# Optimization experiments

Hardware: AMD Instinct MI355X
Metric: run time of the kernel (lower is better)

## Reference

```python
import jax, jax.numpy as jnp
import numpy as np
import math

B, S, OBS, ACT = 64, 256, 96, 29
D, H, L, FF = 512, 8, 8, 2048
HD = D // H
EPS = 1e-5

def _ln(x, g, b):
    m = jnp.mean(x, axis=-1, keepdims=True)
    v = jnp.mean((x - m) ** 2, axis=-1, keepdims=True)
    return (x - m) * jax.lax.rsqrt(v + EPS) * g + b

def _pos_encoding():
    pos = jnp.arange(S, dtype=jnp.float32)[:, None]
    div = jnp.exp(jnp.arange(0, D, 2, dtype=jnp.float32) * (-math.log(10000.0) / D))
    pe = jnp.zeros((S, D), dtype=jnp.float32)
    pe = pe.at[:, 0::2].set(jnp.sin(pos * div))
    pe = pe.at[:, 1::2].set(jnp.cos(pos * div))
    return pe

def setup_inputs() -> dict:
    key = jax.random.key(0)
    ks = iter(jax.random.split(key, 64))
    def w(shape, scale=0.02):
        return jax.random.normal(next(ks), shape, dtype=jnp.float32) * scale
    inp = {
        "observations": jax.random.normal(next(ks), (B, S, OBS), dtype=jnp.float32),
        "W_in": w((OBS, D)), "b_in": jnp.zeros((D,)),
        "g_in": jnp.ones((D,)), "be_in": jnp.zeros((D,)),
        "Wq": w((L, D, D)), "bq": jnp.zeros((L, D)),
        "Wk": w((L, D, D)), "bk": jnp.zeros((L, D)),
        "Wv": w((L, D, D)), "bv": jnp.zeros((L, D)),
        "Wo": w((L, D, D)), "bo": jnp.zeros((L, D)),
        "g1": jnp.ones((L, D)), "be1": jnp.zeros((L, D)),
        "W1": w((L, D, FF)), "b1": jnp.zeros((L, FF)),
        "W2": w((L, FF, D)), "b2": jnp.zeros((L, D)),
        "g2": jnp.ones((L, D)), "be2": jnp.zeros((L, D)),
        "Wp1": w((D, D // 2)), "bp1": jnp.zeros((D // 2,)),
        "gp1": jnp.ones((D // 2,)), "bep1": jnp.zeros((D // 2,)),
        "Wp2": w((D // 2, D // 4)), "bp2": jnp.zeros((D // 4,)),
        "gp2": jnp.ones((D // 4,)), "bep2": jnp.zeros((D // 4,)),
        "Wp3": w((D // 4, ACT)), "bp3": jnp.zeros((ACT,)),
        "action_scale": jnp.ones((ACT,)), "action_bias": jnp.zeros((ACT,)),
    }
    return inp

def _forward(observations, W_in, b_in, g_in, be_in, Wq, bq, Wk, bk, Wv, bv, Wo, bo,
             g1, be1, W1, b1, W2, b2, g2, be2,
             Wp1, bp1, gp1, bep1, Wp2, bp2, gp2, bep2, Wp3, bp3,
             action_scale, action_bias):
    gelu = lambda x: jax.nn.gelu(x, approximate=False)
    # input projection + LN + GELU (dropout = identity in eval)
    x = gelu(_ln(observations @ W_in + b_in, g_in, be_in))
    x = x + _pos_encoding()[None, :, :]  # [B,S,D]
    scale = 1.0 / math.sqrt(HD)
    for l in range(L):
        q = (x @ Wq[l] + bq[l]).reshape(B, S, H, HD)
        k = (x @ Wk[l] + bk[l]).reshape(B, S, H, HD)
        v = (x @ Wv[l] + bv[l]).reshape(B, S, H, HD)
        scores = jnp.einsum('bqhd,bkhd->bhqk', q, k) * scale
        attn = jax.nn.softmax(scores, axis=-1)
        o = jnp.einsum('bhqk,bkhd->bqhd', attn, v).reshape(B, S, D)
        x = _ln(x + (o @ Wo[l] + bo[l]), g1[l], be1[l])
        h = gelu(x @ W1[l] + b1[l])
        x = _ln(x + (h @ W2[l] + b2[l]), g2[l], be2[l])
    y = gelu(_ln(x @ Wp1 + bp1, gp1, bep1))
    y = gelu(_ln(y @ Wp2 + bp2, gp2, bep2))
    actions = jnp.tanh(y @ Wp3 + bp3)
    return actions * action_scale + action_bias

def reference(observations, W_in, b_in, g_in, be_in, Wq, bq, Wk, bk, Wv, bv, Wo, bo,
              g1, be1, W1, b1, W2, b2, g2, be2,
              Wp1, bp1, gp1, bep1, Wp2, bp2, gp2, bep2, Wp3, bp3,
              action_scale, action_bias):
    return _forward(observations, W_in, b_in, g_in, be_in, Wq, bq, Wk, bk, Wv, bv, Wo, bo,
                    g1, be1, W1, b1, W2, b2, g2, be2,
                    Wp1, bp1, gp1, bep1, Wp2, bp2, gp2, bep2, Wp3, bp3,
                    action_scale, action_bias)
```

## Files before the change

### kernel.cpp

```cpp
#include <hip/hip_runtime.h>

typedef unsigned short u16;
typedef unsigned int u32;
typedef __attribute__((ext_vector_type(8))) __bf16 bf16x8;
typedef __attribute__((ext_vector_type(4))) float f32x4;
typedef __attribute__((ext_vector_type(2))) float f32x2;

#define B_ 64
#define S_ 256
#define OBS_ 96
#define ACT_ 29
#define D_ 512
#define H_ 8
#define L_ 8
#define FF_ 2048
#define HD_ 64
#define NTOK (B_ * S_)
#define QKV3 (3 * D_)

__device__ __forceinline__ u16 f2bf(float f) {
    __bf16 h = (__bf16)f;
    u16 u; __builtin_memcpy(&u, &h, 2); return u;
}
__device__ __forceinline__ float bf2f(u16 h) {
    return __uint_as_float(((u32)h) << 16);
}
__device__ __forceinline__ u16 f2h(float f) {
    _Float16 h = (_Float16)f;
    u16 u; __builtin_memcpy(&u, &h, 2); return u;
}
__device__ __forceinline__ float h2f(u16 u) {
    _Float16 h; __builtin_memcpy(&h, &u, 2); return (float)h;
}
__device__ __forceinline__ float gelu_f(float x) {
    const float k1 = 2.3022121f;
    const float k2 = 0.10294451f;
    float x2 = x * x;
    float arg = x * __builtin_fmaf(x2, k2, k1);
    float e = exp2f(arg);
    float r = __builtin_amdgcn_rcpf(1.0f + e);
    return __builtin_fmaf(-x, r, x);
}
__device__ __forceinline__ f32x2 gelu2(f32x2 x) {
    const float k1 = 2.3022121f;
    const float k2 = 0.10294451f;
    f32x2 x2 = x * x;
    f32x2 arg = x * (x2 * k2 + k1);
    f32x2 e;
    e.x = exp2f(arg.x);
    e.y = exp2f(arg.y);
    f32x2 one_e = e + 1.0f;
    f32x2 r;
    r.x = __builtin_amdgcn_rcpf(one_e.x);
    r.y = __builtin_amdgcn_rcpf(one_e.y);
    return x - x * r;
}
__device__ __forceinline__ void gld_lds16(const u16* g, u16* l) {
    __builtin_amdgcn_global_load_lds(
        (const __attribute__((address_space(1))) unsigned int*)g,
        (__attribute__((address_space(3))) unsigned int*)l, 16, 0, 0);
}

__global__ __launch_bounds__(256) void transpose_bf16_kernel(
    const float* __restrict__ src, u16* __restrict__ dst, int K, int N,
    size_t srcStride, size_t dstStride)
{
    __shared__ float tile[32][33];
    int n0 = blockIdx.x * 32, k0 = blockIdx.y * 32;
    const float* s = src + (size_t)blockIdx.z * srcStride;
    u16* d = dst + (size_t)blockIdx.z * dstStride;
    int tx = threadIdx.x, ty = threadIdx.y;
    for (int i = 0; i < 32; i += 8)
        tile[ty + i][tx] = s[(size_t)(k0 + ty + i) * N + n0 + tx];
    __syncthreads();
    for (int i = 0; i < 32; i += 8)
        d[(size_t)(n0 + ty + i) * K + k0 + tx] = f2bf(tile[tx][ty + i]);
}

__global__ __launch_bounds__(256) void concat_bias_kernel(
    const float* __restrict__ bq, const float* __restrict__ bk,
    const float* __restrict__ bv, float* __restrict__ dst)
{
    int i = blockIdx.x * 256 + threadIdx.x;
    int l = i / QKV3, r = i - l * QKV3;
    float v;
    if (r < D_)            v = bq[l * D_ + r];
    else if (r < 2 * D_)   v = bk[l * D_ + r - D_];
    else                   v = bv[l * D_ + r - 2 * D_];
    dst[i] = v;
}

__global__ __launch_bounds__(256) void in_gemm_kernel(
    const float* __restrict__ obs, const float* __restrict__ Win,
    const float* __restrict__ b_in, float* __restrict__ outp)
{
    __shared__ float As[OBS_][68];
    __shared__ float Bs[OBS_][68];
    int m0 = blockIdx.y * 64, n0 = blockIdx.x * 64;
    int t = threadIdx.x;
    #pragma unroll
    for (int i = 0; i < 24; i++) {
        int idx = i * 256 + t;
        int m = idx / OBS_, kk = idx - m * OBS_;
        As[kk][m] = obs[(size_t)(m0 + m) * OBS_ + kk];
    }
    #pragma unroll
    for (int i = 0; i < 24; i++) {
        int idx = i * 256 + t;
        int kk = idx >> 6, n = idx & 63;
        Bs[kk][n] = Win[(size_t)kk * D_ + n0 + n];
    }
    __syncthreads();
    int tm = t >> 4, tn = t & 15;
    float acc[4][4] = {};
    for (int kk = 0; kk < OBS_; kk++) {
        float4 a = *(const float4*)&As[kk][tm * 4];
        float4 b = *(const float4*)&Bs[kk][tn * 4];
        const float av[4] = {a.x, a.y, a.z, a.w};
        const float bv[4] = {b.x, b.y, b.z, b.w};
        #pragma unroll
        for (int r = 0; r < 4; r++)
            #pragma unroll
            for (int c = 0; c < 4; c++) acc[r][c] += av[r] * bv[c];
    }
    #pragma unroll
    for (int r = 0; r < 4; r++)
        #pragma unroll
        for (int c = 0; c < 4; c++) {
            int col = n0 + tn * 4 + c;
            outp[(size_t)(m0 + tm * 4 + r) * D_ + col] = acc[r][c] + b_in[col];
        }
}

template <int EPI, int TN, bool SPLITK>
__global__ __launch_bounds__(256, 3) void gemm_bt_kernel(
    const u16* __restrict__ A, const u16* __restrict__ BT,
    const float* __restrict__ bias, void* __restrict__ C,
    void* __restrict__ C2, int M, int N, int K, int kLen)
{
    constexpr int NI = TN / 32;
    constexpr int BCH = TN / 64;
    constexpr int ABUF = 128 * 32;
    constexpr int BBUF = TN * 32;
    __shared__ __align__(16) u16 smem[2 * ABUF + 2 * BBUF];
    int bx = blockIdx.x;
    int m0 = (bx & 127) * 128, n0 = (bx >> 7) * TN;
    int z = SPLITK ? blockIdx.z : 0;
    int kStart = z * kLen;
    int t = threadIdx.x;
    int lane = t & 63, w = t >> 6;
    int wm = w >> 1, wn = w & 1;
    int l15 = lane & 15, quad = lane >> 4;

    int offA[2], offB[BCH];
    #pragma unroll
    for (int i = 0; i < 2; i++) {
        int ci = t + i * 256;
        int r = ci >> 2, s = ci & 3, gc = s ^ ((r ^ (r >> 2)) & 3);
        offA[i] = r * K + gc * 8;
    }
    #pragma unroll
    for (int i = 0; i < BCH; i++) {
        int ci = t + i * 256;
        int r = ci >> 2, s = ci & 3, gc = s ^ ((r ^ (r >> 2)) & 3);
        offB[i] = r * K + gc * 8;
    }
    const u16* Ag = A + (size_t)m0 * K + kStart;
    const u16* Bg = BT + (size_t)n0 * K + kStart;

    int aoff[4], boff[NI];
    #pragma unroll
    for (int mi = 0; mi < 4; mi++) {
        int row = wm * 64 + mi * 16 + l15;
        aoff[mi] = row * 32 + ((quad ^ ((row ^ (row >> 2)) & 3)) * 8);
    }
    #pragma unroll
    for (int ni = 0; ni < NI; ni++) {
        int row = wn * (TN / 2) + ni * 16 + l15;
        boff[ni] = row * 32 + ((quad ^ ((row ^ (row >> 2)) & 3)) * 8);
    }

    f32x4 acc[4][NI];
    f32x4 zero = {0.f, 0.f, 0.f, 0.f};
    #pragma unroll
    for (int mi = 0; mi < 4; mi++)
        #pragma unroll
        for (int ni = 0; ni < NI; ni++) acc[mi][ni] = zero;

    auto stage = [&](int buf, int kt) {
        const u16* Ab = Ag + kt * 32;
        const u16* Bb = Bg + kt * 32;
        u16* dA = smem + buf * ABUF;
        u16* dB = smem + 2 * ABUF + buf * BBUF;
        #pragma unroll
        for (int i = 0; i < 2; i++) gld_lds16(Ab + offA[i], dA + (t + i * 256) * 8);
        #pragma unroll
        for (int i = 0; i < BCH; i++) gld_lds16(Bb + offB[i], dB + (t + i * 256) * 8);
    };

    int nk = kLen >> 5;
    stage(0, 0);
    for (int kt = 0; kt < nk; ++kt) {
        int cur = kt & 1;
        __syncthreads();
        if (kt + 1 < nk) stage(cur ^ 1, kt + 1);
        const u16* As = smem + cur * ABUF;
        const u16* Bs = smem + 2 * ABUF + cur * BBUF;
        bf16x8 a[4], b[NI];
        #pragma unroll
        for (int mi = 0; mi < 4; mi++)
            a[mi] = *(const bf16x8*)&As[aoff[mi]];
        #pragma unroll
        for (int ni = 0; ni < NI; ni++)
            b[ni] = *(const bf16x8*)&Bs[boff[ni]];
        #pragma unroll
        for (int mi = 0; mi < 4; mi++)
            #pragma unroll
            for (int ni = 0; ni < NI; ni++)
                acc[mi][ni] = __builtin_amdgcn_mfma_f32_16x16x32_bf16(
                    a[mi], b[ni], acc[mi][ni], 0, 0, 0);
    }

    bool partial = SPLITK && (z == 1);
    if (EPI == 2) {
        #pragma unroll
        for (int ni = 0; ni < NI; ni++) {
            int col = n0 + wn * (TN / 2) + ni * 16 + l15;
            float bv = partial ? 0.f : bias[col];
            #pragma unroll
            for (int mi = 0; mi < 4; mi++) {
                int rbase = m0 + wm * 64 + mi * 16 + quad * 4;
                f32x4 v = acc[mi][ni];
                #pragma unroll
                for (int r = 0; r < 4; r++)
                    ((float*)C)[(size_t)(rbase + r) * N + col] = v[r] + bv;
            }
        }
    } else {
        __syncthreads();
        u16* Ct = smem;
        #pragma unroll
        for (int ni = 0; ni < NI; ni++) {
            int colt = wn * (TN / 2) + ni * 16 + l15;
            float bv = partial ? 0.f : bias[n0 + colt];
            #pragma unroll
            for (int mi = 0; mi < 4; mi++) {
                int rbase = wm * 64 + mi * 16 + quad * 4;
                f32x4 v = acc[mi][ni];
                f32x2 y01 = {v[0], v[1]};
                f32x2 y23 = {v[2], v[3]};
                y01 = y01 + bv;
                y23 = y23 + bv;
                if (EPI == 1) { y01 = gelu2(y01); y23 = gelu2(y23); }
                const float ys[4] = {y01.x, y01.y, y23.x, y23.y};
                #pragma unroll
                for (int r = 0; r < 4; r++) {
                    u16 hv = (EPI == 3) ? f2h(ys[r]) : f2bf(ys[r]);
                    int row = rbase + r;
                    int cc = colt >> 3;
                    Ct[row * TN + (((cc ^ (row & 7)) * 8) | (colt & 7))] = hv;
                }
            }
        }
        __syncthreads();
        u16* dst = partial ? (u16*)C2 : (u16*)C;
        constexpr int CPR = TN / 8;
        #pragma unroll
        for (int i = 0; i < TN / 16; i++) {
            int ch = t + i * 256;
            int row = ch / CPR, cc = ch % CPR;
            uint4 vv = *(const uint4*)&Ct[row * TN + ((cc ^ (row & 7)) * 8)];
            *(uint4*)(dst + (size_t)(m0 + row) * N + n0 + cc * 8) = vv;
        }
    }
}

__global__ __launch_bounds__(256) void attn_kernel(
    const u16* __restrict__ qkv, u16* __restrict__ o)
{
    __shared__ __align__(16) u16 kvs[S_ * HD_];
    __shared__ __align__(16) u16 P[4 * 16 * S_];
    int bx = blockIdx.x;
    int qc = bx & 3;
    int h = (bx >> 2) & 7;
    int b = bx >> 5;
    int t = threadIdx.x;
    int lane = t & 63, w = t >> 6;
    int l15 = lane & 15, quad = lane >> 4;
    size_t rowb = (size_t)b * S_;

    {
        const u16* src = qkv + (rowb + t) * QKV3 + D_ + h * HD_;
        int sw = t & 7;
        #pragma unroll
        for (int j = 0; j < 8; j++)
            *(uint4*)&kvs[t * HD_ + ((j ^ sw) * 8)] = *(const uint4*)(src + j * 8);
    }
    bf16x8 aQ[2];
    {
        int qrow = qc * 64 + w * 16 + l15;
        const u16* src = qkv + (rowb + qrow) * QKV3 + h * HD_ + quad * 8;
        aQ[0] = *(const bf16x8*)(src);
        aQ[1] = *(const bf16x8*)(src + 32);
    }
    __syncthreads();

    f32x4 sc[16];
    #pragma unroll
    for (int nc = 0; nc < 16; nc++) {
        f32x4 acc = {0.f, 0.f, 0.f, 0.f};
        int row = nc * 16 + l15;
        int s0 = quad ^ (row & 7);
        bf16x8 b0 = *(const bf16x8*)&kvs[row * HD_ + s0 * 8];
        bf16x8 b1 = *(const bf16x8*)&kvs[row * HD_ + (s0 ^ 4) * 8];
        acc = __builtin_amdgcn_mfma_f32_16x16x32_bf16(aQ[0], b0, acc, 0, 0, 0);
        acc = __builtin_amdgcn_mfma_f32_16x16x32_bf16(aQ[1], b1, acc, 0, 0, 0);
        sc[nc] = acc;
    }
    const float scale = 0.125f;
    float rmax[4], rinv[4];
    #pragma unroll
    for (int r = 0; r < 4; r++) {
        float mx = -1e30f;
        #pragma unroll
        for (int nc = 0; nc < 16; nc++) mx = fmaxf(mx, sc[nc][r]);
        for (int off = 1; off < 16; off <<= 1) mx = fmaxf(mx, __shfl_xor(mx, off));
        rmax[r] = mx * scale;
    }
    #pragma unroll
    for (int r = 0; r < 4; r++) {
        float sum = 0.f;
        #pragma unroll
        for (int nc = 0; nc < 16; nc++) {
            float p = __expf(sc[nc][r] * scale - rmax[r]);
            sc[nc][r] = p;
            sum += p;
        }
        for (int off = 1; off < 16; off <<= 1) sum += __shfl_xor(sum, off);
        rinv[r] = 1.0f / sum;
    }
    #pragma unroll
    for (int nc = 0; nc < 16; nc++)
        #pragma unroll
        for (int r = 0; r < 4; r++) {
            int prow = quad * 4 + r;
            int col = nc * 16 + l15;
            int slot = (col >> 3) ^ (prow & 7);
            P[w * 4096 + prow * 256 + slot * 8 + (col & 7)] = f2bf(sc[nc][r]);
        }
    __syncthreads();

    {
        const u16* src = qkv + (rowb + t) * QKV3 + 2 * D_ + h * HD_;
        int chunkc = t >> 3, bytec = t & 7;
        #pragma unroll
        for (int dj = 0; dj < 8; dj++) {
            uint4 x = *(const uint4*)(src + dj * 8);
            const u16* xs = (const u16*)&x;
            #pragma unroll
            for (int i = 0; i < 8; i++) {
                int vrow = dj * 8 + i;
                kvs[vrow * 256 + ((chunkc ^ (vrow & 7)) * 8) + bytec] = xs[i];
            }
        }
    }
    __syncthreads();

    f32x4 accO[4];
    f32x4 zero = {0.f, 0.f, 0.f, 0.f};
    #pragma unroll
    for (int nt = 0; nt < 4; nt++) accO[nt] = zero;
    for (int ks = 0; ks < 8; ks++) {
        int ch = ks * 4 + quad;
        bf16x8 aP = *(const bf16x8*)&P[w * 4096 + l15 * 256 + ((ch ^ (l15 & 7)) * 8)];
        #pragma unroll
        for (int nt = 0; nt < 4; nt++) {
            int vrow = nt * 16 + l15;
            bf16x8 bV = *(const bf16x8*)&kvs[vrow * 256 + ((ch ^ (vrow & 7)) * 8)];
            accO[nt] = __builtin_amdgcn_mfma_f32_16x16x32_bf16(aP, bV, accO[nt], 0, 0, 0);
        }
    }
    __syncthreads();
    u16* Ot = P;
    #pragma unroll
    for (int nt = 0; nt < 4; nt++)
        #pragma unroll
        for (int r = 0; r < 4; r++) {
            int row = w * 16 + quad * 4 + r;
            int col = nt * 16 + l15;
            int cc = col >> 3;
            Ot[row * 64 + (((cc ^ (row & 7)) * 8) | (col & 7))] =
                f2bf(accO[nt][r] * rinv[r]);
        }
    __syncthreads();
    #pragma unroll
    for (int i = 0; i < 2; i++) {
        int ch = t + i * 256;
        int row = ch >> 3, cc = ch & 7;
        uint4 vv = *(const uint4*)&Ot[row * 64 + ((cc ^ (row & 7)) * 8)];
        *(uint4*)(o + (rowb + qc * 64 + row) * D_ + h * HD_ + cc * 8) = vv;
    }
}

template <int WIDTH, int INK, bool RES, bool GELU, bool PE, bool SUM2>
__global__ __launch_bounds__(256) void ln_kernel(
    const void* __restrict__ in, const void* __restrict__ in2,
    const u16* __restrict__ res,
    const float* __restrict__ g, const float* __restrict__ b,
    u16* __restrict__ out)
{
    constexpr int T = WIDTH / 4;
    constexpr int R = 256 / T;
    __shared__ float rs[R][2], rq[R][2];
    int t = threadIdx.x;
    int r = t / T, j = t % T;
    int row = blockIdx.x * R + r;
    size_t base = (size_t)row * WIDTH + j * 4;
    float v[4];
    if (INK == 0) {
        float4 x = *(const float4*)((const float*)in + base);
        v[0] = x.x; v[1] = x.y; v[2] = x.z; v[3] = x.w;
    } else {
        uint2 x = *(const uint2*)((const u16*)in + base);
        const u16* xs = (const u16*)&x;
        #pragma unroll
        for (int i = 0; i < 4; i++) v[i] = h2f(xs[i]);
    }
    if (SUM2) {
        if (INK == 0) {
            float4 x = *(const float4*)((const float*)in2 + base);
            v[0] += x.x; v[1] += x.y; v[2] += x.z; v[3] += x.w;
        } else {
            uint2 x = *(const uint2*)((const u16*)in2 + base);
            const u16* xs = (const u16*)&x;
            #pragma unroll
            for (int i = 0; i < 4; i++) v[i] += h2f(xs[i]);
        }
    }
    if (RES) {
        uint2 x = *(const uint2*)(res + base);
        const u16* xs = (const u16*)&x;
        #pragma unroll
        for (int i = 0; i < 4; i++) v[i] += bf2f(xs[i]);
    }
    float sm = v[0] + v[1] + v[2] + v[3];
    float sq = v[0] * v[0] + v[1] * v[1] + v[2] * v[2] + v[3] * v[3];
    if constexpr (T >= 64) {
        #pragma unroll
        for (int off = 32; off; off >>= 1) {
            sm += __shfl_xor(sm, off);
            sq += __shfl_xor(sq, off);
        }
    } else {
        #pragma unroll
        for (int off = 16; off; off >>= 1) {
            sm += __shfl_xor(sm, off, 32);
            sq += __shfl_xor(sq, off, 32);
        }
    }
    if constexpr (T == 128) {
        if ((t & 63) == 0) { rs[r][(t >> 6) & 1] = sm; rq[r][(t >> 6) & 1] = sq; }
        __syncthreads();
        sm = rs[r][0] + rs[r][1];
        sq = rq[r][0] + rq[r][1];
    }
    float mean = sm / (float)WIDTH;
    float var = sq / (float)WIDTH - mean * mean;
    float rstd = rsqrtf(var + 1e-5f);
    float4 gv = *(const float4*)(g + j * 4);
    float4 bv = *(const float4*)(b + j * 4);
    const float gs[4] = {gv.x, gv.y, gv.z, gv.w};
    const float bs[4] = {bv.x, bv.y, bv.z, bv.w};
    u16 o4[4];
    #pragma unroll
    for (int i = 0; i < 4; i++) {
        float y = (v[i] - mean) * rstd * gs[i] + bs[i];
        if (GELU) y = gelu_f(y);
        if (PE) {
            const float c = -9.210340371976184f / (float)D_;
            int s = row & (S_ - 1);
            int col = j * 4 + i;
            int i2 = col >> 1;
            float ang = (float)s * __expf((float)(2 * i2) * c);
            y += (col & 1) ? __cosf(ang) : __sinf(ang);
        }
        o4[i] = f2bf(y);
    }
    uint2 ov;
    ov.x = (u32)o4[0] | ((u32)o4[1] << 16);
    ov.y = (u32)o4[2] | ((u32)o4[3] << 16);
    *(uint2*)(out + base) = ov;
}

__global__ __launch_bounds__(256) void head_kernel(
    const u16* __restrict__ y2, const float* __restrict__ W,
    const float* __restrict__ bias, const float* __restrict__ scl,
    const float* __restrict__ bs, float* __restrict__ out)
{
    __shared__ float Ws[128 * ACT_];
    __shared__ u16 Ys[8 * 128];
    int t = threadIdx.x;
    for (int i = t; i < 128 * ACT_; i += 256) Ws[i] = W[i];
    int r0 = blockIdx.x * 8;
    for (int i = t; i < 8 * 128; i += 256) Ys[i] = y2[(size_t)r0 * 128 + i];
    __syncthreads();
    int lr = t >> 5, c = t & 31;
    if (c < ACT_) {
        float acc = bias[c];
        for (int kk = 0; kk < 128; kk++)
            acc += bf2f(Ys[lr * 128 + kk]) * Ws[kk * ACT_ + c];
        float y = tanhf(acc);
        out[(size_t)(r0 + lr) * ACT_ + c] = y * scl[c] + bs[c];
    }
}

extern "C" void kernel_launch(void* const* d_in, const int* in_sizes, int n_in,
                              void* d_out, int out_size, void* d_ws, size_t ws_size,
                              hipStream_t stream)
{
    const float* obs   = (const float*)d_in[0];
    const float* W_in  = (const float*)d_in[1];
    const float* b_in  = (const float*)d_in[2];
    const float* g_in  = (const float*)d_in[3];
    const float* be_in = (const float*)d_in[4];
    const float* Wq  = (const float*)d_in[5];
    const float* bq  = (const float*)d_in[6];
    const float* Wk  = (const float*)d_in[7];
    const float* bk  = (const float*)d_in[8];
    const float* Wv  = (const float*)d_in[9];
    const float* bv  = (const float*)d_in[10];
    const float* Wo  = (const float*)d_in[11];
    const float* bo  = (const float*)d_in[12];
    const float* g1  = (const float*)d_in[13];
    const float* be1 = (const float*)d_in[14];
    const float* W1  = (const float*)d_in[15];
    const float* b1  = (const float*)d_in[16];
    const float* W2  = (const float*)d_in[17];
    const float* b2  = (const float*)d_in[18];
    const float* g2  = (const float*)d_in[19];
    const float* be2 = (const float*)d_in[20];
    const float* Wp1  = (const float*)d_in[21];
    const float* bp1  = (const float*)d_in[22];
    const float* gp1  = (const float*)d_in[23];
    const float* bep1 = (const float*)d_in[24];
    const float* Wp2  = (const float*)d_in[25];
    const float* bp2  = (const float*)d_in[26];
    const float* gp2  = (const float*)d_in[27];
    const float* bep2 = (const float*)d_in[28];
    const float* Wp3  = (const float*)d_in[29];
    const float* bp3  = (const float*)d_in[30];
    const float* ascl = (const float*)d_in[31];
    const float* abias = (const float*)d_in[32];

    char* ws = (char*)d_ws;
    size_t off = 0;
    auto alloc = [&](size_t bytes) {
        void* p = ws + off;
        off += (bytes + 255) & ~(size_t)255;
        return p;
    };
    u16* WQKVT = (u16*)alloc((size_t)L_ * QKV3 * D_ * 2);
    u16* WOT   = (u16*)alloc((size_t)L_ * D_ * D_ * 2);
    u16* W1T   = (u16*)alloc((size_t)L_ * D_ * FF_ * 2);
    u16* W2T   = (u16*)alloc((size_t)L_ * FF_ * D_ * 2);
    u16* WP1T  = (u16*)alloc((size_t)D_ * (D_ / 2) * 2);
    u16* WP2T  = (u16*)alloc((size_t)(D_ / 2) * (D_ / 4) * 2);
    float* bqkv = (float*)alloc((size_t)L_ * QKV3 * 4);
    u16* x_bf = (u16*)alloc((size_t)NTOK * D_ * 2);
    float* tmp = (float*)alloc((size_t)NTOK * D_ * 4);
    char* regionA = (char*)alloc((size_t)NTOK * FF_ * 2);
    size_t base_need = off;
    char* tmp2 = ws + base_need;
    bool split = (ws_size >= base_need + (size_t)NTOK * D_ * 2);
    (void)in_sizes; (void)n_in; (void)out_size;

    u16* qkvbuf = (u16*)(regionA);
    u16* obuf = (u16*)(regionA + (size_t)NTOK * QKV3 * 2);
    u16* hbuf = (u16*)(regionA);
    u16* y1_bf = (u16*)(regionA);
    u16* y2_bf = (u16*)(regionA + (32u << 20));

    dim3 tb(32, 8);
    size_t DD = (size_t)D_ * D_;
    transpose_bf16_kernel<<<dim3(16, 16, L_), tb, 0, stream>>>(
        Wq, WQKVT, D_, D_, DD, (size_t)QKV3 * D_);
    transpose_bf16_kernel<<<dim3(16, 16, L_), tb, 0, stream>>>(
        Wk, WQKVT + DD, D_, D_, DD, (size_t)QKV3 * D_);
    transpose_bf16_kernel<<<dim3(16, 16, L_), tb, 0, stream>>>(
        Wv, WQKVT + 2 * DD, D_, D_, DD, (size_t)QKV3 * D_);
    transpose_bf16_kernel<<<dim3(16, 16, L_), tb, 0, stream>>>(
        Wo, WOT, D_, D_, DD, DD);
    transpose_bf16_kernel<<<dim3(64, 16, L_), tb, 0, stream>>>(
        W1, W1T, D_, FF_, (size_t)D_ * FF_, (size_t)D_ * FF_);
    transpose_bf16_kernel<<<dim3(16, 64, L_), tb, 0, stream>>>(
        W2, W2T, FF_, D_, (size_t)D_ * FF_, (size_t)D_ * FF_);
    transpose_bf16_kernel<<<dim3(8, 16, 1), tb, 0, stream>>>(
        Wp1, WP1T, D_, D_ / 2, 0, 0);
    transpose_bf16_kernel<<<dim3(4, 8, 1), tb, 0, stream>>>(
        Wp2, WP2T, D_ / 2, D_ / 4, 0, 0);
    concat_bias_kernel<<<L_ * QKV3 / 256, 256, 0, stream>>>(bq, bk, bv, bqkv);

    in_gemm_kernel<<<dim3(D_ / 64, NTOK / 64), 256, 0, stream>>>(
        obs, W_in, b_in, tmp);
    ln_kernel<D_, 0, false, true, true, false><<<NTOK / 2, 256, 0, stream>>>(
        tmp, nullptr, nullptr, g_in, be_in, x_bf);

    const int MG = NTOK / 128;
    for (int l = 0; l < L_; l++) {
        const u16* wqkvt = WQKVT + (size_t)l * QKV3 * D_;
        const u16* wot = WOT + (size_t)l * DD;
        const u16* w1t = W1T + (size_t)l * D_ * FF_;
        const u16* w2t = W2T + (size_t)l * FF_ * D_;

        gemm_bt_kernel<0, 128, false><<<MG * (QKV3 / 128), 256, 0, stream>>>(
            x_bf, wqkvt, bqkv + l * QKV3, qkvbuf, nullptr, NTOK, QKV3, D_, D_);
        attn_kernel<<<B_ * H_ * (S_ / 64), 256, 0, stream>>>(qkvbuf, obuf);
        if (split) {
            gemm_bt_kernel<3, 128, true><<<dim3(MG * 4, 1, 2), 256, 0, stream>>>(
                obuf, wot, bo + l * D_, tmp, tmp2, NTOK, D_, D_, D_ / 2);
            ln_kernel<D_, 1, true, false, false, true><<<NTOK / 2, 256, 0, stream>>>(
                tmp, tmp2, x_bf, g1 + l * D_, be1 + l * D_, x_bf);
        } else {
            gemm_bt_kernel<2, 128, false><<<MG * 4, 256, 0, stream>>>(
                obuf, wot, bo + l * D_, tmp, nullptr, NTOK, D_, D_, D_);
            ln_kernel<D_, 0, true, false, false, false><<<NTOK / 2, 256, 0, stream>>>(
                tmp, nullptr, x_bf, g1 + l * D_, be1 + l * D_, x_bf);
        }
        gemm_bt_kernel<1, 128, false><<<MG * (FF_ / 128), 256, 0, stream>>>(
            x_bf, w1t, b1 + l * FF_, hbuf, nullptr, NTOK, FF_, D_, D_);
        if (split) {
            gemm_bt_kernel<3, 128, true><<<dim3(MG * 4, 1, 2), 256, 0, stream>>>(
                hbuf, w2t, b2 + l * D_, tmp, tmp2, NTOK, D_, FF_, FF_ / 2);
            ln_kernel<D_, 1, true, false, false, true><<<NTOK / 2, 256, 0, stream>>>(
                tmp, tmp2, x_bf, g2 + l * D_, be2 + l * D_, x_bf);
        } else {
            gemm_bt_kernel<2, 128, false><<<MG * 4, 256, 0, stream>>>(
                hbuf, w2t, b2 + l * D_, tmp, nullptr, NTOK, D_, FF_, FF_);
            ln_kernel<D_, 0, true, false, false, false><<<NTOK / 2, 256, 0, stream>>>(
                tmp, nullptr, x_bf, g2 + l * D_, be2 + l * D_, x_bf);
        }
    }

    if (split) {
        gemm_bt_kernel<3, 64, true><<<dim3(MG * 4, 1, 2), 256, 0, stream>>>(
            x_bf, WP1T, bp1, tmp, tmp2, NTOK, D_ / 2, D_, D_ / 2);
        ln_kernel<D_ / 2, 1, false, true, false, true><<<NTOK / 4, 256, 0, stream>>>(
            tmp, tmp2, nullptr, gp1, bep1, y1_bf);
        gemm_bt_kernel<3, 64, true><<<dim3(MG * 2, 1, 2), 256, 0, stream>>>(
            y1_bf, WP2T, bp2, tmp, tmp2, NTOK, D_ / 4, D_ / 2, D_ / 4);
        ln_kernel<D_ / 4, 1, false, true, false, true><<<NTOK / 8, 256, 0, stream>>>(
            tmp, tmp2, nullptr, gp2, bep2, y2_bf);
    } else {
        gemm_bt_kernel<2, 64, false><<<MG * 4, 256, 0, stream>>>(
            x_bf, WP1T, bp1, tmp, nullptr, NTOK, D_ / 2, D_, D_);
        ln_kernel<D_ / 2, 0, false, true, false, false><<<NTOK / 4, 256, 0, stream>>>(
            tmp, nullptr, nullptr, gp1, bep1, y1_bf);
        gemm_bt_kernel<2, 64, false><<<MG * 2, 256, 0, stream>>>(
            y1_bf, WP2T, bp2, tmp, nullptr, NTOK, D_ / 4, D_ / 2, D_ / 2);
        ln_kernel<D_ / 4, 0, false, true, false, false><<<NTOK / 8, 256, 0, stream>>>(
            tmp, nullptr, nullptr, gp2, bep2, y2_bf);
    }
    head_kernel<<<NTOK / 8, 256, 0, stream>>>(
        y2_bf, Wp3, bp3, ascl, abias, (float*)d_out);
}
```

Measured before the change: 2.060 ms.

## Triple-buffer GEMM LDS with vmcnt waits; prefetch V and coalesce K loads in attention

The GEMM moves from double- to triple-buffered shared memory, keeping two tiles in flight. Each step waits on vmcnt for the current tile and uses a single barrier, so global-to-LDS loads overlap more compute. The attention kernel loads V into registers at kernel start to hide its latency behind QK/softmax, and loads K with a lane layout where consecutive threads read contiguous chunks of a row. The costs are more LDS per block, which may lower GEMM occupancy, and more register pressure in attention.

```diff
diff --git a/kernel.cpp b/kernel.cpp
--- a/kernel.cpp
+++ b/kernel.cpp
@@ -139,10 +139,13 @@
     void* __restrict__ C2, int M, int N, int K, int kLen)
 {
     constexpr int NI = TN / 32;
+    constexpr int ACH = 2;
     constexpr int BCH = TN / 64;
+    constexpr int LPT = ACH + BCH;
     constexpr int ABUF = 128 * 32;
     constexpr int BBUF = TN * 32;
-    __shared__ __align__(16) u16 smem[2 * ABUF + 2 * BBUF];
+    constexpr int BUF = ABUF + BBUF;
+    __shared__ __align__(16) u16 smem[3 * BUF];
     int bx = blockIdx.x;
     int m0 = (bx & 127) * 128, n0 = (bx >> 7) * TN;
     int z = SPLITK ? blockIdx.z : 0;
@@ -152,9 +155,9 @@
     int wm = w >> 1, wn = w & 1;
     int l15 = lane & 15, quad = lane >> 4;
 
-    int offA[2], offB[BCH];
-    #pragma unroll
-    for (int i = 0; i < 2; i++) {
+    int offA[ACH], offB[BCH];
+    #pragma unroll
+    for (int i = 0; i < ACH; i++) {
         int ci = t + i * 256;
         int r = ci >> 2, s = ci & 3, gc = s ^ ((r ^ (r >> 2)) & 3);
         offA[i] = r * K + gc * 8;
@@ -187,32 +190,39 @@
         #pragma unroll
         for (int ni = 0; ni < NI; ni++) acc[mi][ni] = zero;
 
-    auto stage = [&](int buf, int kt) {
+    auto stage = [&](int kt) {
+        int bf = kt % 3;
         const u16* Ab = Ag + kt * 32;
         const u16* Bb = Bg + kt * 32;
-        u16* dA = smem + buf * ABUF;
-        u16* dB = smem + 2 * ABUF + buf * BBUF;
-        #pragma unroll
-        for (int i = 0; i < 2; i++) gld_lds16(Ab + offA[i], dA + (t + i * 256) * 8);
+        u16* dA = smem + bf * BUF;
+        u16* dB = dA + ABUF;
+        #pragma unroll
+        for (int i = 0; i < ACH; i++) gld_lds16(Ab + offA[i], dA + (t + i * 256) * 8);
         #pragma unroll
         for (int i = 0; i < BCH; i++) gld_lds16(Bb + offB[i], dB + (t + i * 256) * 8);
     };
 
     int nk = kLen >> 5;
-    stage(0, 0);
+    stage(0);
+    if (nk > 1) stage(1);
     for (int kt = 0; kt < nk; ++kt) {
-        int cur = kt & 1;
-        __syncthreads();
-        if (kt + 1 < nk) stage(cur ^ 1, kt + 1);
-        const u16* As = smem + cur * ABUF;
-        const u16* Bs = smem + 2 * ABUF + cur * BBUF;
+        if (kt + 1 < nk) {
+            asm volatile("s_waitcnt vmcnt(%0)" :: "i"(LPT) : "memory");
+        } else {
+            asm volatile("s_waitcnt vmcnt(0)" ::: "memory");
+        }
+        __builtin_amdgcn_sched_barrier(0);
+        __builtin_amdgcn_s_barrier();
+        if (kt + 2 < nk) stage(kt + 2);
+        const u16* As_ = smem + (kt % 3) * BUF;
+        const u16* Bs_ = As_ + ABUF;
         bf16x8 a[4], b[NI];
         #pragma unroll
         for (int mi = 0; mi < 4; mi++)
-            a[mi] = *(const bf16x8*)&As[aoff[mi]];
+            a[mi] = *(const bf16x8*)&As_[aoff[mi]];
         #pragma unroll
         for (int ni = 0; ni < NI; ni++)
-            b[ni] = *(const bf16x8*)&Bs[boff[ni]];
+            b[ni] = *(const bf16x8*)&Bs_[boff[ni]];
         #pragma unroll
         for (int mi = 0; mi < 4; mi++)
             #pragma unroll
@@ -289,12 +299,21 @@
     int l15 = lane & 15, quad = lane >> 4;
     size_t rowb = (size_t)b * S_;
 
+    uint4 vreg[8];
     {
-        const u16* src = qkv + (rowb + t) * QKV3 + D_ + h * HD_;
-        int sw = t & 7;
-        #pragma unroll
-        for (int j = 0; j < 8; j++)
-            *(uint4*)&kvs[t * HD_ + ((j ^ sw) * 8)] = *(const uint4*)(src + j * 8);
+        const u16* src = qkv + (rowb + t) * QKV3 + 2 * D_ + h * HD_;
+        #pragma unroll
+        for (int dj = 0; dj < 8; dj++) vreg[dj] = *(const uint4*)(src + dj * 8);
+    }
+    {
+        int chunk = t & 7, row0 = t >> 3;
+        #pragma unroll
+        for (int j = 0; j < 8; j++) {
+            int row = row0 + j * 32;
+            const u16* src = qkv + (rowb + row) * QKV3 + D_ + h * HD_ + chunk * 8;
+            *(uint4*)&kvs[row * HD_ + ((chunk ^ (row & 7)) * 8)] =
+                *(const uint4*)src;
+        }
     }
     bf16x8 aQ[2];
     {
@@ -351,12 +370,10 @@
     __syncthreads();
 
     {
-        const u16* src = qkv + (rowb + t) * QKV3 + 2 * D_ + h * HD_;
         int chunkc = t >> 3, bytec = t & 7;
         #pragma unroll
         for (int dj = 0; dj < 8; dj++) {
-            uint4 x = *(const uint4*)(src + dj * 8);
-            const u16* xs = (const u16*)&x;
+            const u16* xs = (const u16*)&vreg[dj];
             #pragma unroll
             for (int i = 0; i < 8; i++) {
                 int vrow = dj * 8 + i;
```

Result: faster. 2.008 ms (-2.5%).
